# Kernel tuning notes

Hardware: AMD Instinct MI355X
Metric: run time of the kernel (lower is better)

The kernel has to match this reference:

```python
import jax, jax.numpy as jnp
import numpy as np

HID = 128   # hidden_size
EDGE = 16   # edge_size
L = 3       # n_layers
K = 3       # sparse_k
U = 4       # atoms per block (uniform)
NB = 20000  # number of blocks
N = NB * U  # number of atoms
EB = 30000  # number of block-level edges


def _egnn_forward(H, Z, edges, edge_attr,
                  emb_in_w, emb_in_b, emb_out_w, emb_out_b,
                  edge_w1, edge_b1, edge_w2, edge_b2,
                  node_w1, node_b1, node_w2, node_b2,
                  coord_w1, coord_b1, coord_w2):
    # ---- sparse-k atom edges from block edges (uniform U atoms per block) ----
    off = jnp.arange(U)
    src_atoms = edges[0][:, None] * U + off            # [EB, U]
    dst_atoms = edges[1][:, None] * U + off            # [EB, U]
    # squared distances between every src/dst atom pair of each block edge
    d2 = jnp.sum((Z[src_atoms][:, :, None, :] - Z[dst_atoms][:, None, :, :]) ** 2, -1)  # [EB,U,U]
    _, idx = jax.lax.top_k(-d2, K)                     # K nearest dst atoms per src atom
    row = jnp.broadcast_to(src_atoms[:, :, None], (EB, U, K)).reshape(-1)   # [E]
    col = jnp.take_along_axis(jnp.broadcast_to(dst_atoms[:, None, :], (EB, U, U)), idx, axis=2).reshape(-1)
    edge_id = jnp.broadcast_to(jnp.arange(EB)[:, None, None], (EB, U, K)).reshape(-1)
    eattr = edge_attr[edge_id]                         # gather block-edge attr per atom edge [E, EDGE]

    # ---- EGNN (Satorras egnn_clean: SiLU, residual h, mean coord agg) ----
    h = H @ emb_in_w + emb_in_b
    x = Z
    ones = jnp.ones((row.shape[0], 1), Z.dtype)
    cnt = jnp.clip(jax.ops.segment_sum(ones, row, num_segments=N), 1.0)
    for l in range(L):
        diff = x[row] - x[col]                         # [E,3]
        radial = jnp.sum(diff * diff, -1, keepdims=True)
        m = jnp.concatenate([h[row], h[col], radial, eattr], -1)   # [E, 2*HID+1+EDGE]
        m = jax.nn.silu(m @ edge_w1[l] + edge_b1[l])
        m = jax.nn.silu(m @ edge_w2[l] + edge_b2[l])   # edge messages [E, HID]
        # coordinate update (mean aggregation over outgoing edges of row)
        w = jax.nn.silu(m @ coord_w1[l] + coord_b1[l]) @ coord_w2[l]   # [E,1]
        x = x + jax.ops.segment_sum(diff * w, row, num_segments=N) / cnt
        # node update (sum aggregation, residual)
        agg = jax.ops.segment_sum(m, row, num_segments=N)
        hn = jnp.concatenate([h, agg], -1)
        h = h + (jax.nn.silu(hn @ node_w1[l] + node_b1[l]) @ node_w2[l] + node_b2[l])
    h = h @ emb_out_w + emb_out_b
    return h, x


def setup_inputs() -> dict:
    key = jax.random.key(0)
    ks = jax.random.split(key, 16)
    s = 0.05
    p = {}
    p["H"] = jax.random.normal(ks[0], (N, HID), jnp.float32)
    p["Z"] = jax.random.normal(ks[1], (N, 3), jnp.float32) * 3.0
    p["block_id"] = jnp.repeat(jnp.arange(NB, dtype=jnp.int32), U)
    p["batch_id"] = jnp.zeros((N,), jnp.int32)
    p["edges"] = jax.random.randint(ks[2], (2, EB), 0, NB, dtype=jnp.int32)
    p["edge_attr"] = jax.random.normal(ks[3], (EB, EDGE), jnp.float32)
    p["emb_in_w"] = jax.random.normal(ks[4], (HID, HID), jnp.float32) * s
    p["emb_in_b"] = jnp.zeros((HID,), jnp.float32)
    p["emb_out_w"] = jax.random.normal(ks[5], (HID, HID), jnp.float32) * s
    p["emb_out_b"] = jnp.zeros((HID,), jnp.float32)
    p["edge_w1"] = jax.random.normal(ks[6], (L, 2 * HID + 1 + EDGE, HID), jnp.float32) * s
    p["edge_b1"] = jnp.zeros((L, HID), jnp.float32)
    p["edge_w2"] = jax.random.normal(ks[7], (L, HID, HID), jnp.float32) * s
    p["edge_b2"] = jnp.zeros((L, HID), jnp.float32)
    p["node_w1"] = jax.random.normal(ks[8], (L, 2 * HID, HID), jnp.float32) * s
    p["node_b1"] = jnp.zeros((L, HID), jnp.float32)
    p["node_w2"] = jax.random.normal(ks[9], (L, HID, HID), jnp.float32) * s
    p["node_b2"] = jnp.zeros((L, HID), jnp.float32)
    p["coord_w1"] = jax.random.normal(ks[10], (L, HID, HID), jnp.float32) * s
    p["coord_b1"] = jnp.zeros((L, HID), jnp.float32)
    p["coord_w2"] = jax.random.normal(ks[11], (L, HID, 1), jnp.float32) * s
    return p


def reference(H, Z, block_id, batch_id, edges, edge_attr,
              emb_in_w, emb_in_b, emb_out_w, emb_out_b,
              edge_w1, edge_b1, edge_w2, edge_b2,
              node_w1, node_b1, node_w2, node_b2,
              coord_w1, coord_b1, coord_w2):
    # block_id / batch_id are carried for API fidelity; uniform-U block layout is static.
    return _egnn_forward(H, Z, edges, edge_attr,
                         emb_in_w, emb_in_b, emb_out_w, emb_out_b,
                         edge_w1, edge_b1, edge_w2, edge_b2,
                         node_w1, node_b1, node_w2, node_b2,
                         coord_w1, coord_b1, coord_w2)
```

## Files before the change

### kernel.cpp

```cpp
#include <hip/hip_runtime.h>
#include <math.h>

#define HIDC 128
#define EDGEF 16
#define LAY 3
#define KNN 3
#define UU 4
#define NBLK 20000
#define NATOM (NBLK*UU)
#define EBK 30000
#define EALL (EBK*UU*KNN)
#define NGRP (EBK*UU)

#define W1F_L 36864
#define W2F_L 16384
#define NW1F_L 32768

#define E_WG 16
#define ROWS_WG (E_WG*12)
#define WAVES_WG 12

typedef __attribute__((ext_vector_type(8))) short bf16x8;
typedef __attribute__((ext_vector_type(4))) float f32x4;

__device__ __forceinline__ float silu_f(float v) {
    return __fdividef(v, 1.0f + __expf(-v));
}

__device__ __forceinline__ unsigned short f2bf(float f) {
    union { float f; unsigned int u; } v; v.f = f;
    unsigned int r = v.u + 0x7FFFu + ((v.u >> 16) & 1u);
    return (unsigned short)(r >> 16);
}

__device__ __forceinline__ float bf2f(unsigned short h) {
    union { unsigned int u; float f; } t; t.u = ((unsigned int)h) << 16;
    return t.f;
}

__device__ __forceinline__ void split2(float v, short& hi, short& lo) {
    unsigned short h = f2bf(v);
    hi = (short)h;
    lo = (short)f2bf(v - bf2f(h));
}

__device__ __forceinline__ void csplit(float v, unsigned short& hi, unsigned short& lo) {
    unsigned int hu = __float_as_uint(v) & 0xffff0000u;
    hi = (unsigned short)(hu >> 16);
    lo = f2bf(v - __uint_as_float(hu));
}

__device__ __forceinline__ unsigned int cvtpk2(float a, float b) {
    unsigned int r;
    asm("v_cvt_pk_bf16_f32 %0, %1, %2" : "=v"(r) : "v"(a), "v"(b));
    return r;
}

__device__ __forceinline__ void stage16(const unsigned short* gsrc, unsigned short* ldst) {
    __builtin_amdgcn_global_load_lds(
        (const __attribute__((address_space(1))) unsigned int*)(const void*)gsrc,
        (__attribute__((address_space(3))) unsigned int*)(void*)ldst,
        16, 0, 0);
}


__global__ void k_count(const int* __restrict__ edges, int* __restrict__ degB) {
    int e = blockIdx.x * 256 + threadIdx.x;
    if (e < EBK) atomicAdd(&degB[edges[e]], 1);
}

__global__ void k_scan(const int* __restrict__ degB, int* __restrict__ offB) {
    __shared__ int s[1024];
    __shared__ int carry;
    if (threadIdx.x == 0) carry = 0;
    __syncthreads();
    for (int base = 0; base < NBLK; base += 1024) {
        int i = base + threadIdx.x;
        int v = (i < NBLK) ? degB[i] : 0;
        s[threadIdx.x] = v;
        __syncthreads();
        for (int d = 1; d < 1024; d <<= 1) {
            int t = (threadIdx.x >= d) ? s[threadIdx.x - d] : 0;
            __syncthreads();
            s[threadIdx.x] += t;
            __syncthreads();
        }
        if (i < NBLK) offB[i] = carry + s[threadIdx.x] - v;
        int tot = s[1023];
        __syncthreads();
        if (threadIdx.x == 0) carry += tot;
        __syncthreads();
    }
    if (threadIdx.x == 0) offB[NBLK] = carry;
}

__global__ void k_fill(const int* __restrict__ edges, const int* __restrict__ offB,
                       int* __restrict__ cursor, int* __restrict__ listE) {
    int e = blockIdx.x * 256 + threadIdx.x;
    if (e < EBK) {
        int b = edges[e];
        int p = atomicAdd(&cursor[b], 1);
        listE[offB[b] + p] = e;
    }
}

__global__ void k_topk(const int* __restrict__ edges, const float* __restrict__ Z,
                       int* __restrict__ colIdx) {
    int t = blockIdx.x * 256 + threadIdx.x;
    if (t >= EBK * UU) return;
    int e = t >> 2, u = t & 3;
    int b0 = edges[e], b1 = edges[EBK + e];
    int s = b0 * UU + u;
    float zs0 = Z[s*3+0], zs1 = Z[s*3+1], zs2 = Z[s*3+2];
    float d2[UU];
    #pragma unroll
    for (int v = 0; v < UU; v++) {
        int d = b1 * UU + v;
        float a0 = __fsub_rn(zs0, Z[d*3+0]);
        float a1 = __fsub_rn(zs1, Z[d*3+1]);
        float a2 = __fsub_rn(zs2, Z[d*3+2]);
        float p0 = __fmul_rn(a0, a0);
        float p1 = __fmul_rn(a1, a1);
        float p2 = __fmul_rn(a2, a2);
        d2[v] = __fadd_rn(__fadd_rn(p0, p1), p2);
    }
    bool used[UU] = {false, false, false, false};
    #pragma unroll
    for (int k = 0; k < KNN; k++) {
        int best = -1;
        float bd = INFINITY;
        #pragma unroll
        for (int v = 0; v < UU; v++) {
            if (!used[v] && d2[v] < bd) { bd = d2[v]; best = v; }
        }
        used[best] = true;
        colIdx[t * KNN + k] = b1 * UU + best;
    }
}


__global__ void k_wfrag(const float* __restrict__ ew1, const float* __restrict__ ew2,
                        const float* __restrict__ cw1,
                        const float* __restrict__ nw1, const float* __restrict__ nw2,
                        unsigned short* __restrict__ w1f_hi, unsigned short* __restrict__ w1f_lo,
                        unsigned short* __restrict__ w2f_hi, unsigned short* __restrict__ w2f_lo,
                        unsigned short* __restrict__ c1f_hi, unsigned short* __restrict__ c1f_lo,
                        unsigned short* __restrict__ n1f_hi, unsigned short* __restrict__ n1f_lo,
                        unsigned short* __restrict__ n2f_hi, unsigned short* __restrict__ n2f_lo) {
    int i = blockIdx.x * 256 + threadIdx.x;
    float v = 0.f;
    unsigned short* dh = nullptr;
    unsigned short* dl = nullptr;
    int di = 0;
    if (i < 3 * W1F_L) {
        int l = i / W1F_L, rem = i % W1F_L;
        int chunk = rem >> 9, lane = (rem >> 3) & 63, t = rem & 7;
        int kb = chunk >> 3, j = chunk & 7;
        int k = kb*32 + (lane >> 4)*8 + t, n = j*16 + (lane & 15);
        v = (k < 273) ? ew1[(size_t)l*273*128 + (size_t)k*128 + n] : 0.f;
        dh = w1f_hi; dl = w1f_lo; di = i;
    } else {
        int i2 = i - 3 * W1F_L;
        if (i2 < 3 * W2F_L) {
            int l = i2 / W2F_L, rem = i2 % W2F_L;
            int chunk = rem >> 9, lane = (rem >> 3) & 63, t = rem & 7;
            int kb = chunk >> 3, j = chunk & 7;
            int k = kb*32 + (lane >> 4)*8 + t, n = j*16 + (lane & 15);
            v = ew2[(size_t)l*128*128 + (size_t)k*128 + n];
            dh = w2f_hi; dl = w2f_lo; di = i2;
        } else {
            int i3 = i2 - 3 * W2F_L;
            if (i3 < 3 * W2F_L) {
                int l = i3 / W2F_L, rem = i3 % W2F_L;
                int chunk = rem >> 9, lane = (rem >> 3) & 63, t = rem & 7;
                int kb = chunk >> 3, j = chunk & 7;
                int k = kb*32 + (lane >> 4)*8 + t, n = j*16 + (lane & 15);
                v = cw1[(size_t)l*128*128 + (size_t)k*128 + n];
                dh = c1f_hi; dl = c1f_lo; di = i3;
            } else {
                int i4 = i3 - 3 * W2F_L;
                if (i4 < 3 * NW1F_L) {
                    int l = i4 / NW1F_L, rem = i4 % NW1F_L;
                    int chunk = rem >> 9, lane = (rem >> 3) & 63, t = rem & 7;
                    int kb = chunk >> 3, j = chunk & 7;
                    int k = kb*32 + (lane >> 4)*8 + t, n = j*16 + (lane & 15);
                    v = nw1[(size_t)l*256*128 + (size_t)k*128 + n];
                    dh = n1f_hi; dl = n1f_lo; di = i4;
                } else {
                    int i5 = i4 - 3 * NW1F_L;
                    if (i5 >= 3 * W2F_L) return;
                    int l = i5 / W2F_L, rem = i5 % W2F_L;
                    int chunk = rem >> 9, lane = (rem >> 3) & 63, t = rem & 7;
                    int kb = chunk >> 3, j = chunk & 7;
                    int k = kb*32 + (lane >> 4)*8 + t, n = j*16 + (lane & 15);
                    v = nw2[(size_t)l*128*128 + (size_t)k*128 + n];
                    dh = n2f_hi; dl = n2f_lo; di = i5;
                }
            }
        }
    }
    short hi, lo;
    split2(v, hi, lo);
    dh[di] = (unsigned short)hi;
    dl[di] = (unsigned short)lo;
}


__global__ __launch_bounds__(768, 6) void k_edge_flat(
    const unsigned short* __restrict__ hHI,
    const unsigned short* __restrict__ hLO,
    const float* __restrict__ x,
    const float* __restrict__ eattr,
    const int* __restrict__ edges0,
    const int* __restrict__ colIdx,
    const unsigned short* __restrict__ w1f_hi, const unsigned short* __restrict__ w1f_lo,
    const unsigned short* __restrict__ w2f_hi, const unsigned short* __restrict__ w2f_lo,
    const unsigned short* __restrict__ c1f_hi, const unsigned short* __restrict__ c1f_lo,
    const float* __restrict__ eb1,
    const float* __restrict__ eb2,
    const float* __restrict__ cb1,
    const float* __restrict__ cw2v,
    unsigned short* __restrict__ msum,
    float* __restrict__ xsum)
{
    __shared__ unsigned short wbufH[4096], wbufL[4096];
    __shared__ unsigned short Mlds[ROWS_WG * 128];
    __shared__ float diffLDS[ROWS_WG][3];
    __shared__ float pLDS[ROWS_WG];

    const int tid = threadIdx.x;
    const int wid = tid >> 6, l = tid & 63;
    const int g = l >> 4, er = l & 15;
    const int e_base = blockIdx.x * E_WG;
    const int r0 = wid * 16;

    const int row_g = r0 + er;
    const int e_loc = row_g / 12;
    const int rr = row_g - e_loc * 12;
    const int u = rr / 3;
    const int kk = rr - u * 3;
    const int e = e_base + e_loc;
    const int bs = edges0[e];
    const int srcA = bs * 4 + u;
    const int colA = colIdx[(e * 4 + u) * 3 + kk];
    float rad = 0.f;
    if (g == 0) {
        float dx = x[srcA*3+0] - x[colA*3+0];
        float dy = x[srcA*3+1] - x[colA*3+1];
        float dz = x[srcA*3+2] - x[colA*3+2];
        rad = dx*dx + dy*dy + dz*dz;
        diffLDS[row_g][0] = dx; diffLDS[row_g][1] = dy; diffLDS[row_g][2] = dz;
    }

    const int goff = wid * 512 + l * 8;
    unsigned short* lb0H = wbufH + wid * 512;
    unsigned short* lb1H = wbufH + 2048 + wid * 512;
    unsigned short* lb0L = wbufL + wid * 512;
    unsigned short* lb1L = wbufL + 2048 + wid * 512;

    {
        f32x4 acc[8];
        #pragma unroll
        for (int jj = 0; jj < 8; jj++) acc[jj] = (f32x4){0.f, 0.f, 0.f, 0.f};

        #pragma unroll 1
        for (int kb = 0; kb < 9; kb++) {
            __syncthreads();
            if (wid < 4) {
                stage16(w1f_hi + (kb << 12) + goff,        lb0H);
                stage16(w1f_hi + (kb << 12) + 2048 + goff, lb1H);
                stage16(w1f_lo + (kb << 12) + goff,        lb0L);
                stage16(w1f_lo + (kb << 12) + 2048 + goff, lb1L);
            }
            bf16x8 ah, al;
            if (kb < 8) {
                const size_t off = (kb < 4) ? ((size_t)srcA * 128 + kb * 32 + g * 8)
                                            : ((size_t)colA * 128 + (kb - 4) * 32 + g * 8);
                ah = *(const bf16x8*)(hHI + off);
                al = *(const bf16x8*)(hLO + off);
            } else {
                float tv[8];
                #pragma unroll
                for (int q = 0; q < 8; q++) tv[q] = 0.f;
                if (g == 0) {
                    tv[0] = rad;
                    #pragma unroll
                    for (int q = 1; q < 8; q++) tv[q] = eattr[(size_t)e*16 + (q-1)];
                } else if (g == 1) {
                    #pragma unroll
                    for (int q = 0; q < 8; q++) tv[q] = eattr[(size_t)e*16 + 7 + q];
                } else if (g == 2) {
                    tv[0] = eattr[(size_t)e*16 + 15];
                }
                #pragma unroll
                for (int q = 0; q < 8; q++) { unsigned short hh, ll; csplit(tv[q], hh, ll); ah[q] = (short)hh; al[q] = (short)ll; }
            }
            __syncthreads();
            __builtin_amdgcn_s_setprio(1);
            #pragma unroll
            for (int jj = 0; jj < 8; jj++) {
                const int off = (jj << 9) + (l << 3);
                bf16x8 wh = *(const bf16x8*)&wbufH[off];
                bf16x8 wl = *(const bf16x8*)&wbufL[off];
                acc[jj] = __builtin_amdgcn_mfma_f32_16x16x32_bf16(ah, wh, acc[jj], 0, 0, 0);
                acc[jj] = __builtin_amdgcn_mfma_f32_16x16x32_bf16(al, wh, acc[jj], 0, 0, 0);
                acc[jj] = __builtin_amdgcn_mfma_f32_16x16x32_bf16(ah, wl, acc[jj], 0, 0, 0);
            }
            __builtin_amdgcn_s_setprio(0);
        }
        #pragma unroll
        for (int jp = 0; jp < 4; jp++) {
            const int n0 = (jp * 2) * 16 + er, n1 = n0 + 16;
            const float b0 = eb1[n0], b1 = eb1[n1];
            #pragma unroll
            for (int reg = 0; reg < 4; reg++) {
                const int row = r0 + g * 4 + reg;
                float v0 = silu_f(acc[jp*2][reg] + b0);
                float v1 = silu_f(acc[jp*2+1][reg] + b1);
                unsigned int pk = cvtpk2(v0, v1);
                const int m = (row & 7) << 3;
                Mlds[row * 128 + (n0 ^ m)] = (unsigned short)pk;
                Mlds[row * 128 + (n1 ^ m)] = (unsigned short)(pk >> 16);
            }
        }
    }

    {
        f32x4 acc[8];
        #pragma unroll
        for (int jj = 0; jj < 8; jj++) acc[jj] = (f32x4){0.f, 0.f, 0.f, 0.f};

        #pragma unroll 1
        for (int kb = 0; kb < 4; kb++) {
            __syncthreads();
            if (wid < 4) {
                stage16(w2f_hi + (kb << 12) + goff,        lb0H);
                stage16(w2f_hi + (kb << 12) + 2048 + goff, lb1H);
                stage16(w2f_lo + (kb << 12) + goff,        lb0L);
                stage16(w2f_lo + (kb << 12) + 2048 + goff, lb1L);
            }
            const int aoff = row_g * 128 + ((kb * 32 + g * 8) ^ ((row_g & 7) << 3));
            bf16x8 a2 = *(const bf16x8*)&Mlds[aoff];
            __syncthreads();
            __builtin_amdgcn_s_setprio(1);
            #pragma unroll
            for (int jj = 0; jj < 8; jj++) {
                const int off = (jj << 9) + (l << 3);
                bf16x8 wh = *(const bf16x8*)&wbufH[off];
                bf16x8 wl = *(const bf16x8*)&wbufL[off];
                acc[jj] = __builtin_amdgcn_mfma_f32_16x16x32_bf16(a2, wh, acc[jj], 0, 0, 0);
                acc[jj] = __builtin_amdgcn_mfma_f32_16x16x32_bf16(a2, wl, acc[jj], 0, 0, 0);
            }
            __builtin_amdgcn_s_setprio(0);
        }
        #pragma unroll
        for (int jp = 0; jp < 4; jp++) {
            const int n0 = (jp * 2) * 16 + er, n1 = n0 + 16;
            const float b0 = eb2[n0], b1 = eb2[n1];
            #pragma unroll
            for (int reg = 0; reg < 4; reg++) {
                const int row = r0 + g * 4 + reg;
                float v0 = silu_f(acc[jp*2][reg] + b0);
                float v1 = silu_f(acc[jp*2+1][reg] + b1);
                unsigned int pk = cvtpk2(v0, v1);
                const int m = (row & 7) << 3;
                Mlds[row * 128 + (n0 ^ m)] = (unsigned short)pk;
                Mlds[row * 128 + (n1 ^ m)] = (unsigned short)(pk >> 16);
            }
        }
    }

    {
        f32x4 acc[8];
        #pragma unroll
        for (int jj = 0; jj < 8; jj++) acc[jj] = (f32x4){0.f, 0.f, 0.f, 0.f};

        #pragma unroll 1
        for (int kb = 0; kb < 4; kb++) {
            __syncthreads();
            if (wid < 4) {
                stage16(c1f_hi + (kb << 12) + goff,        lb0H);
                stage16(c1f_hi + (kb << 12) + 2048 + goff, lb1H);
                stage16(c1f_lo + (kb << 12) + goff,        lb0L);
                stage16(c1f_lo + (kb << 12) + 2048 + goff, lb1L);
            }
            const int aoff = row_g * 128 + ((kb * 32 + g * 8) ^ ((row_g & 7) << 3));
            bf16x8 a3 = *(const bf16x8*)&Mlds[aoff];
            __syncthreads();
            __builtin_amdgcn_s_setprio(1);
            #pragma unroll
            for (int jj = 0; jj < 8; jj++) {
                const int off = (jj << 9) + (l << 3);
                bf16x8 wh = *(const bf16x8*)&wbufH[off];
                bf16x8 wl = *(const bf16x8*)&wbufL[off];
                acc[jj] = __builtin_amdgcn_mfma_f32_16x16x32_bf16(a3, wh, acc[jj], 0, 0, 0);
                acc[jj] = __builtin_amdgcn_mfma_f32_16x16x32_bf16(a3, wl, acc[jj], 0, 0, 0);
            }
            __builtin_amdgcn_s_setprio(0);
        }
        float p[4] = {0.f, 0.f, 0.f, 0.f};
        #pragma unroll
        for (int jj = 0; jj < 8; jj++) {
            const int n = jj * 16 + er;
            const float cb = cb1[n], cw = cw2v[n];
            #pragma unroll
            for (int reg = 0; reg < 4; reg++)
                p[reg] += silu_f(acc[jj][reg] + cb) * cw;
        }
        #pragma unroll
        for (int d = 1; d < 16; d <<= 1) {
            #pragma unroll
            for (int reg = 0; reg < 4; reg++)
                p[reg] += __shfl_xor(p[reg], d);
        }
        if (er == 0) {
            #pragma unroll
            for (int reg = 0; reg < 4; reg++)
                pLDS[r0 + g * 4 + reg] = p[reg];
        }
    }
    __syncthreads();

    for (int t = tid; t < E_WG * 4 * 64; t += 768) {
        const int gi = t >> 6, cp = t & 63;
        const int c0 = cp * 2;
        const int el = gi >> 2, uu2 = gi & 3;
        const int base = el * 12 + uu2 * 3;
        float s0 = 0.f, s1 = 0.f;
        #pragma unroll
        for (int k3 = 0; k3 < 3; k3++) {
            const int row = base + k3;
            const int m = (row & 7) << 3;
            unsigned int pr = *(const unsigned int*)&Mlds[row * 128 + (c0 ^ m)];
            s0 += bf2f((unsigned short)(pr & 0xffffu));
            s1 += bf2f((unsigned short)(pr >> 16));
        }
        ((unsigned int*)msum)[(size_t)((e_base + el) * 4 + uu2) * 64 + cp] = cvtpk2(s0, s1);
    }
    if (tid < E_WG * 4 * 3) {
        const int gi = tid / 3, c = tid - gi * 3;
        const int el = gi >> 2, uu2 = gi & 3;
        const int base = el * 12 + uu2 * 3;
        float xs = 0.f;
        #pragma unroll
        for (int k3 = 0; k3 < 3; k3++)
            xs += diffLDS[base + k3][c] * pLDS[base + k3];
        xsum[(size_t)((e_base + el) * 4 + uu2) * 3 + c] = xs;
    }
}


__global__ void k_xupd(const float* __restrict__ xcur, const float* __restrict__ xsum,
                       const int* __restrict__ offB, const int* __restrict__ listE,
                       float* __restrict__ xnext)
{
    int i = blockIdx.x * 256 + threadIdx.x;
    if (i >= NATOM * 3) return;
    int a = i / 3, d = i - a * 3;
    int b = a >> 2, u = a & 3;
    int o0 = offB[b], o1 = offB[b + 1];
    float xs = 0.f;
    for (int pos = o0; pos < o1; pos++) {
        int e = listE[pos];
        xs += xsum[(size_t)(e * 4 + u) * 3 + d];
    }
    int deg = o1 - o0;
    xnext[i] = xcur[i] + ((deg > 0) ? xs / (3.0f * (float)deg) : 0.f);
}


__global__ __launch_bounds__(256, 4) void k_node(
    unsigned short* __restrict__ hHI,
    unsigned short* __restrict__ hLO,
    const unsigned short* __restrict__ msum,
    const int* __restrict__ offB,
    const int* __restrict__ listE,
    const unsigned short* __restrict__ n1f_hi, const unsigned short* __restrict__ n1f_lo,
    const unsigned short* __restrict__ n2f_hi, const unsigned short* __restrict__ n2f_lo,
    const float* __restrict__ nb1,
    const float* __restrict__ nb2)
{
    __shared__ unsigned short wbufH[4096], wbufL[4096];
    __shared__ unsigned short hid[4][16 * 128];

    const int tid = threadIdx.x;
    const int wid = tid >> 6, l = tid & 63;
    const int g = l >> 4, er = l & 15;
    const int a0 = blockIdx.x * 64 + wid * 16;
    const int a = a0 + er;
    const int b = a >> 2, u = a & 3;
    const int o0 = offB[b], o1 = offB[b + 1];

    const int goff = wid * 512 + l * 8;
    unsigned short* lb0H = wbufH + wid * 512;
    unsigned short* lb1H = wbufH + 2048 + wid * 512;
    unsigned short* lb0L = wbufL + wid * 512;
    unsigned short* lb1L = wbufL + 2048 + wid * 512;

    {
        f32x4 acc[8];
        #pragma unroll
        for (int jj = 0; jj < 8; jj++) acc[jj] = (f32x4){0.f, 0.f, 0.f, 0.f};

        #pragma unroll 1
        for (int kb = 0; kb < 8; kb++) {
            __syncthreads();
            stage16(n1f_hi + (kb << 12) + goff,        lb0H);
            stage16(n1f_hi + (kb << 12) + 2048 + goff, lb1H);
            stage16(n1f_lo + (kb << 12) + goff,        lb0L);
            stage16(n1f_lo + (kb << 12) + 2048 + goff, lb1L);
            bf16x8 ah, al;
            if (kb < 4) {
                const size_t off = (size_t)a * 128 + kb * 32 + g * 8;
                ah = *(const bf16x8*)(hHI + off);
                al = *(const bf16x8*)(hLO + off);
            } else {
                float s[8];
                #pragma unroll
                for (int q = 0; q < 8; q++) s[q] = 0.f;
                for (int pos = o0; pos < o1; pos++) {
                    const int e = listE[pos];
                    bf16x8 mv = *(const bf16x8*)(msum + (size_t)(e * 4 + u) * 128 + (kb - 4) * 32 + g * 8);
                    #pragma unroll
                    for (int q = 0; q < 8; q++) s[q] += bf2f((unsigned short)mv[q]);
                }
                #pragma unroll
                for (int q = 0; q < 8; q++) { unsigned short hh, ll; csplit(s[q], hh, ll); ah[q] = (short)hh; al[q] = (short)ll; }
            }
            __syncthreads();
            __builtin_amdgcn_s_setprio(1);
            #pragma unroll
            for (int jj = 0; jj < 8; jj++) {
                const int off = (jj << 9) + (l << 3);
                bf16x8 wh = *(const bf16x8*)&wbufH[off];
                bf16x8 wl = *(const bf16x8*)&wbufL[off];
                acc[jj] = __builtin_amdgcn_mfma_f32_16x16x32_bf16(ah, wh, acc[jj], 0, 0, 0);
                acc[jj] = __builtin_amdgcn_mfma_f32_16x16x32_bf16(al, wh, acc[jj], 0, 0, 0);
                acc[jj] = __builtin_amdgcn_mfma_f32_16x16x32_bf16(ah, wl, acc[jj], 0, 0, 0);
            }
            __builtin_amdgcn_s_setprio(0);
        }
        #pragma unroll
        for (int jp = 0; jp < 4; jp++) {
            const int n0 = (jp * 2) * 16 + er, n1 = n0 + 16;
            const float b0 = nb1[n0], b1 = nb1[n1];
            #pragma unroll
            for (int reg = 0; reg < 4; reg++) {
                const int row = g * 4 + reg;
                float v0 = silu_f(acc[jp*2][reg] + b0);
                float v1 = silu_f(acc[jp*2+1][reg] + b1);
                unsigned int pk = cvtpk2(v0, v1);
                const int m = (row & 7) << 3;
                hid[wid][row * 128 + (n0 ^ m)] = (unsigned short)pk;
                hid[wid][row * 128 + (n1 ^ m)] = (unsigned short)(pk >> 16);
            }
        }
    }

    {
        f32x4 acc[8];
        #pragma unroll
        for (int jj = 0; jj < 8; jj++) acc[jj] = (f32x4){0.f, 0.f, 0.f, 0.f};

        #pragma unroll 1
        for (int kb = 0; kb < 4; kb++) {
            __syncthreads();
            stage16(n2f_hi + (kb << 12) + goff,        lb0H);
            stage16(n2f_hi + (kb << 12) + 2048 + goff, lb1H);
            stage16(n2f_lo + (kb << 12) + goff,        lb0L);
            stage16(n2f_lo + (kb << 12) + 2048 + goff, lb1L);
            const int aoff = er * 128 + ((kb * 32 + g * 8) ^ ((er & 7) << 3));
            bf16x8 ab = *(const bf16x8*)&hid[wid][aoff];
            __syncthreads();
            __builtin_amdgcn_s_setprio(1);
            #pragma unroll
            for (int jj = 0; jj < 8; jj++) {
                const int off = (jj << 9) + (l << 3);
                bf16x8 wh = *(const bf16x8*)&wbufH[off];
                bf16x8 wl = *(const bf16x8*)&wbufL[off];
                acc[jj] = __builtin_amdgcn_mfma_f32_16x16x32_bf16(ab, wh, acc[jj], 0, 0, 0);
                acc[jj] = __builtin_amdgcn_mfma_f32_16x16x32_bf16(ab, wl, acc[jj], 0, 0, 0);
            }
            __builtin_amdgcn_s_setprio(0);
        }
        #pragma unroll
        for (int jj = 0; jj < 8; jj++) {
            const int n = jj * 16 + er;
            const float bv = nb2[n];
            #pragma unroll
            for (int reg = 0; reg < 4; reg++) {
                const int row = g * 4 + reg;
                const size_t idx = (size_t)(a0 + row) * 128 + n;
                float v = acc[jj][reg] + bv + bf2f(hHI[idx]) + bf2f(hLO[idx]);
                unsigned short hh, ll; csplit(v, hh, ll);
                hHI[idx] = hh;
                hLO[idx] = ll;
            }
        }
    }
}


template<bool PLANEIN, bool PLANEOUT>
__global__ __launch_bounds__(128) void k_gemm(
    const float* __restrict__ A0,
    const unsigned short* __restrict__ AHI, const unsigned short* __restrict__ ALO,
    const float* __restrict__ W, const float* __restrict__ bias,
    float* __restrict__ C,
    unsigned short* __restrict__ CHI, unsigned short* __restrict__ CLO, int M)
{
    __shared__ float At[128][32];
    __shared__ float Bs[32][128];
    const int tid = threadIdx.x;
    const int tile0 = blockIdx.x * 32;
    const int r = tid >> 2, part = tid & 3;
    const int gr = tile0 + r;

    if (gr < M) {
        #pragma unroll
        for (int j = 0; j < 8; j++) {
            int c = part * 32 + j * 4;
            float f0, f1, f2, f3;
            if (PLANEIN) {
                ushort4 vh = *(const ushort4*)(AHI + (size_t)gr * 128 + c);
                ushort4 vl = *(const ushort4*)(ALO + (size_t)gr * 128 + c);
                f0 = bf2f(vh.x) + bf2f(vl.x);
                f1 = bf2f(vh.y) + bf2f(vl.y);
                f2 = bf2f(vh.z) + bf2f(vl.z);
                f3 = bf2f(vh.w) + bf2f(vl.w);
            } else {
                float4 v = *(const float4*)(A0 + (size_t)gr * 128 + c);
                f0 = v.x; f1 = v.y; f2 = v.z; f3 = v.w;
            }
            At[c][r] = f0; At[c+1][r] = f1; At[c+2][r] = f2; At[c+3][r] = f3;
        }
    } else {
        #pragma unroll
        for (int j = 0; j < 8; j++) {
            int c = part * 32 + j * 4;
            At[c][r] = 0.f; At[c+1][r] = 0.f; At[c+2][r] = 0.f; At[c+3][r] = 0.f;
        }
    }

    float acc[4][8];
    #pragma unroll
    for (int i = 0; i < 4; i++)
        #pragma unroll
        for (int j = 0; j < 8; j++) acc[i][j] = 0.f;

    const int tx = tid & 15, ty = tid >> 4;

    for (int kb = 0; kb < 4; kb++) {
        __syncthreads();
        #pragma unroll
        for (int j = 0; j < 8; j++) {
            int li = j * 512 + tid * 4;
            int kk = li >> 7, c = li & 127;
            float4 v = *(const float4*)(W + (size_t)(kb * 32 + kk) * 128 + c);
            *(float4*)&Bs[kk][c] = v;
        }
        __syncthreads();
        #pragma unroll 8
        for (int kk = 0; kk < 32; kk++) {
            float4 a  = *(const float4*)&At[kb * 32 + kk][ty * 4];
            float4 b0 = *(const float4*)&Bs[kk][tx * 8];
            float4 b1 = *(const float4*)&Bs[kk][tx * 8 + 4];
            float av[4] = {a.x, a.y, a.z, a.w};
            float bv[8] = {b0.x, b0.y, b0.z, b0.w, b1.x, b1.y, b1.z, b1.w};
            #pragma unroll
            for (int i = 0; i < 4; i++)
                #pragma unroll
                for (int j = 0; j < 8; j++)
                    acc[i][j] = fmaf(av[i], bv[j], acc[i][j]);
        }
    }

    #pragma unroll
    for (int i = 0; i < 4; i++) {
        int grr = tile0 + ty * 4 + i;
        if (grr >= M) continue;
        #pragma unroll
        for (int j = 0; j < 8; j++) {
            int c = tx * 8 + j;
            float v = acc[i][j] + bias[c];
            if (PLANEOUT) {
                unsigned short hh, ll; csplit(v, hh, ll);
                CHI[(size_t)grr * 128 + c] = hh;
                CLO[(size_t)grr * 128 + c] = ll;
            } else {
                C[(size_t)grr * 128 + c] = v;
            }
        }
    }
}


extern "C" void kernel_launch(void* const* d_in, const int* in_sizes, int n_in,
                              void* d_out, int out_size, void* d_ws, size_t ws_size,
                              hipStream_t stream) {
    const float* H        = (const float*)d_in[0];
    const float* Z        = (const float*)d_in[1];
    const int*   edges    = (const int*)  d_in[4];
    const float* eattr    = (const float*)d_in[5];
    const float* emb_in_w = (const float*)d_in[6];
    const float* emb_in_b = (const float*)d_in[7];
    const float* emb_out_w= (const float*)d_in[8];
    const float* emb_out_b= (const float*)d_in[9];
    const float* edge_w1  = (const float*)d_in[10];
    const float* edge_b1  = (const float*)d_in[11];
    const float* edge_w2  = (const float*)d_in[12];
    const float* edge_b2  = (const float*)d_in[13];
    const float* node_w1  = (const float*)d_in[14];
    const float* node_b1  = (const float*)d_in[15];
    const float* node_w2  = (const float*)d_in[16];
    const float* node_b2  = (const float*)d_in[17];
    const float* coord_w1 = (const float*)d_in[18];
    const float* coord_b1 = (const float*)d_in[19];
    const float* coord_w2 = (const float*)d_in[20];

    float* out  = (float*)d_out;
    float* hbuf = out;
    float* xout = out + (size_t)NATOM * 128;

    char* w = (char*)d_ws;
    unsigned short* hHI = (unsigned short*)w;  w += (size_t)NATOM * 128 * 2;
    unsigned short* hLO = (unsigned short*)w;  w += (size_t)NATOM * 128 * 2;
    unsigned short* msum = (unsigned short*)w; w += (size_t)NGRP * 128 * 2;
    float* xsum = (float*)w;           w += (size_t)NGRP * 3 * 4;
    float* xA  = (float*)w;            w += (size_t)NATOM * 3 * 4;
    float* xB  = (float*)w;            w += (size_t)NATOM * 3 * 4;
    unsigned short* w1f_hi = (unsigned short*)w;  w += (size_t)3 * W1F_L * 2;
    unsigned short* w1f_lo = (unsigned short*)w;  w += (size_t)3 * W1F_L * 2;
    unsigned short* w2f_hi = (unsigned short*)w;  w += (size_t)3 * W2F_L * 2;
    unsigned short* w2f_lo = (unsigned short*)w;  w += (size_t)3 * W2F_L * 2;
    unsigned short* c1f_hi = (unsigned short*)w;  w += (size_t)3 * W2F_L * 2;
    unsigned short* c1f_lo = (unsigned short*)w;  w += (size_t)3 * W2F_L * 2;
    unsigned short* n1f_hi = (unsigned short*)w;  w += (size_t)3 * NW1F_L * 2;
    unsigned short* n1f_lo = (unsigned short*)w;  w += (size_t)3 * NW1F_L * 2;
    unsigned short* n2f_hi = (unsigned short*)w;  w += (size_t)3 * W2F_L * 2;
    unsigned short* n2f_lo = (unsigned short*)w;  w += (size_t)3 * W2F_L * 2;
    int* colIdx = (int*)w;             w += (size_t)EALL * 4;
    int* degB   = (int*)w;             w += (size_t)NBLK * 4;
    int* cursor = (int*)w;             w += (size_t)NBLK * 4;
    int* listE  = (int*)w;             w += (size_t)EBK * 4;
    int* offB   = (int*)w;             w += (size_t)(NBLK + 1) * 4;

    hipMemsetAsync(degB,   0, NBLK * sizeof(int), stream);
    hipMemsetAsync(cursor, 0, NBLK * sizeof(int), stream);

    k_count<<<(EBK + 255) / 256, 256, 0, stream>>>(edges, degB);
    k_scan <<<1, 1024, 0, stream>>>(degB, offB);
    k_fill <<<(EBK + 255) / 256, 256, 0, stream>>>(edges, offB, cursor, listE);
    k_topk <<<(EBK * UU + 255) / 256, 256, 0, stream>>>(edges, Z, colIdx);

    {
        int total = 3 * W1F_L + 3 * W2F_L + 3 * W2F_L + 3 * NW1F_L + 3 * W2F_L;
        k_wfrag<<<(total + 255) / 256, 256, 0, stream>>>(
            edge_w1, edge_w2, coord_w1, node_w1, node_w2,
            w1f_hi, w1f_lo, w2f_hi, w2f_lo, c1f_hi, c1f_lo,
            n1f_hi, n1f_lo, n2f_hi, n2f_lo);
    }

    k_gemm<false, true><<<NATOM / 32, 128, 0, stream>>>(
        H, nullptr, nullptr, emb_in_w, emb_in_b, nullptr, hHI, hLO, NATOM);

    const float* xcur = Z;
    for (int l = 0; l < LAY; l++) {
        float* xnext = (l == 0) ? xA : (l == 1) ? xB : xout;

        k_edge_flat<<<EBK / E_WG, 768, 0, stream>>>(
            hHI, hLO, xcur, eattr, edges, colIdx,
            w1f_hi + (size_t)l * W1F_L, w1f_lo + (size_t)l * W1F_L,
            w2f_hi + (size_t)l * W2F_L, w2f_lo + (size_t)l * W2F_L,
            c1f_hi + (size_t)l * W2F_L, c1f_lo + (size_t)l * W2F_L,
            edge_b1 + l * 128, edge_b2 + l * 128, coord_b1 + l * 128, coord_w2 + l * 128,
            msum, xsum);

        k_xupd<<<(NATOM * 3 + 255) / 256, 256, 0, stream>>>(xcur, xsum, offB, listE, xnext);

        k_node<<<NATOM / 64, 256, 0, stream>>>(
            hHI, hLO, msum, offB, listE,
            n1f_hi + (size_t)l * NW1F_L, n1f_lo + (size_t)l * NW1F_L,
            n2f_hi + (size_t)l * W2F_L, n2f_lo + (size_t)l * W2F_L,
            node_b1 + l * 128, node_b2 + l * 128);

        xcur = xnext;
    }

    k_gemm<true, false><<<NATOM / 32, 128, 0, stream>>>(
        nullptr, hHI, hLO, emb_out_w, emb_out_b, hbuf, nullptr, nullptr, NATOM);
}
```

Measured before the change: 918.7 us.

## Widen node kernel to 12 waves sharing staged weights; vectorize gemm I/O

The node-update kernel now runs 768 threads per block covering 192 atoms, so each weight tile staged into LDS by four waves is reused by twelve waves instead of four, cutting global weight traffic per atom. Tail atoms are bounds-guarded and the hidden activation buffer becomes one shared array. Separately, the dense gemm kernel loads inputs in 8-wide vectors and writes hi/lo bf16 output planes with packed 128-bit stores instead of scalar stores. The larger LDS footprint and block size may reduce how many blocks fit per CU.

```diff
diff --git a/kernel.cpp b/kernel.cpp
--- a/kernel.cpp
+++ b/kernel.cpp
@@ -18,7 +18,7 @@
 
 #define E_WG 16
 #define ROWS_WG (E_WG*12)
-#define WAVES_WG 12
+#define NODE_ROWS 192
 
 typedef __attribute__((ext_vector_type(8))) short bf16x8;
 typedef __attribute__((ext_vector_type(4))) float f32x4;
@@ -469,7 +469,7 @@
 }
 
 
-__global__ __launch_bounds__(256, 4) void k_node(
+__global__ __launch_bounds__(768, 6) void k_node(
     unsigned short* __restrict__ hHI,
     unsigned short* __restrict__ hLO,
     const unsigned short* __restrict__ msum,
@@ -481,15 +481,19 @@
     const float* __restrict__ nb2)
 {
     __shared__ unsigned short wbufH[4096], wbufL[4096];
-    __shared__ unsigned short hid[4][16 * 128];
+    __shared__ unsigned short hid[NODE_ROWS * 128];
 
     const int tid = threadIdx.x;
     const int wid = tid >> 6, l = tid & 63;
     const int g = l >> 4, er = l & 15;
-    const int a0 = blockIdx.x * 64 + wid * 16;
-    const int a = a0 + er;
-    const int b = a >> 2, u = a & 3;
-    const int o0 = offB[b], o1 = offB[b + 1];
+    const int r0 = wid * 16;
+    const int row_g = r0 + er;
+    const int a = blockIdx.x * NODE_ROWS + row_g;
+    const bool aOK = (a < NATOM);
+    const int aC = aOK ? a : 0;
+    const int b = aC >> 2, u = aC & 3;
+    const int o0 = aOK ? offB[b] : 0;
+    const int o1 = aOK ? offB[b + 1] : 0;
 
     const int goff = wid * 512 + l * 8;
     unsigned short* lb0H = wbufH + wid * 512;
@@ -505,13 +509,15 @@
         #pragma unroll 1
         for (int kb = 0; kb < 8; kb++) {
             __syncthreads();
-            stage16(n1f_hi + (kb << 12) + goff,        lb0H);
-            stage16(n1f_hi + (kb << 12) + 2048 + goff, lb1H);
-            stage16(n1f_lo + (kb << 12) + goff,        lb0L);
-            stage16(n1f_lo + (kb << 12) + 2048 + goff, lb1L);
+            if (wid < 4) {
+                stage16(n1f_hi + (kb << 12) + goff,        lb0H);
+                stage16(n1f_hi + (kb << 12) + 2048 + goff, lb1H);
+                stage16(n1f_lo + (kb << 12) + goff,        lb0L);
+                stage16(n1f_lo + (kb << 12) + 2048 + goff, lb1L);
+            }
             bf16x8 ah, al;
             if (kb < 4) {
-                const size_t off = (size_t)a * 128 + kb * 32 + g * 8;
+                const size_t off = (size_t)aC * 128 + kb * 32 + g * 8;
                 ah = *(const bf16x8*)(hHI + off);
                 al = *(const bf16x8*)(hLO + off);
             } else {
@@ -546,13 +552,13 @@
             const float b0 = nb1[n0], b1 = nb1[n1];
             #pragma unroll
             for (int reg = 0; reg < 4; reg++) {
-                const int row = g * 4 + reg;
+                const int row = r0 + g * 4 + reg;
                 float v0 = silu_f(acc[jp*2][reg] + b0);
                 float v1 = silu_f(acc[jp*2+1][reg] + b1);
                 unsigned int pk = cvtpk2(v0, v1);
                 const int m = (row & 7) << 3;
-                hid[wid][row * 128 + (n0 ^ m)] = (unsigned short)pk;
-                hid[wid][row * 128 + (n1 ^ m)] = (unsigned short)(pk >> 16);
+                hid[row * 128 + (n0 ^ m)] = (unsigned short)pk;
+                hid[row * 128 + (n1 ^ m)] = (unsigned short)(pk >> 16);
             }
         }
     }
@@ -565,12 +571,14 @@
         #pragma unroll 1
         for (int kb = 0; kb < 4; kb++) {
             __syncthreads();
-            stage16(n2f_hi + (kb << 12) + goff,        lb0H);
-            stage16(n2f_hi + (kb << 12) + 2048 + goff, lb1H);
-            stage16(n2f_lo + (kb << 12) + goff,        lb0L);
-            stage16(n2f_lo + (kb << 12) + 2048 + goff, lb1L);
-            const int aoff = er * 128 + ((kb * 32 + g * 8) ^ ((er & 7) << 3));
-            bf16x8 ab = *(const bf16x8*)&hid[wid][aoff];
+            if (wid < 4) {
+                stage16(n2f_hi + (kb << 12) + goff,        lb0H);
+                stage16(n2f_hi + (kb << 12) + 2048 + goff, lb1H);
+                stage16(n2f_lo + (kb << 12) + goff,        lb0L);
+                stage16(n2f_lo + (kb << 12) + 2048 + goff, lb1L);
+            }
+            const int aoff = row_g * 128 + ((kb * 32 + g * 8) ^ ((row_g & 7) << 3));
+            bf16x8 ab = *(const bf16x8*)&hid[aoff];
             __syncthreads();
             __builtin_amdgcn_s_setprio(1);
             #pragma unroll
@@ -589,12 +597,15 @@
             const float bv = nb2[n];
             #pragma unroll
             for (int reg = 0; reg < 4; reg++) {
-                const int row = g * 4 + reg;
-                const size_t idx = (size_t)(a0 + row) * 128 + n;
-                float v = acc[jj][reg] + bv + bf2f(hHI[idx]) + bf2f(hLO[idx]);
-                unsigned short hh, ll; csplit(v, hh, ll);
-                hHI[idx] = hh;
-                hLO[idx] = ll;
+                const int row = r0 + g * 4 + reg;
+                const int aw = blockIdx.x * NODE_ROWS + row;
+                if (aw < NATOM) {
+                    const size_t idx = (size_t)aw * 128 + n;
+                    float v = acc[jj][reg] + bv + bf2f(hHI[idx]) + bf2f(hLO[idx]);
+                    unsigned short hh, ll; csplit(v, hh, ll);
+                    hHI[idx] = hh;
+                    hLO[idx] = ll;
+                }
             }
         }
     }
@@ -618,21 +629,20 @@
 
     if (gr < M) {
         #pragma unroll
-        for (int j = 0; j < 8; j++) {
-            int c = part * 32 + j * 4;
-            float f0, f1, f2, f3;
+        for (int j2 = 0; j2 < 4; j2++) {
+            int c = part * 32 + j2 * 8;
             if (PLANEIN) {
-                ushort4 vh = *(const ushort4*)(AHI + (size_t)gr * 128 + c);
-                ushort4 vl = *(const ushort4*)(ALO + (size_t)gr * 128 + c);
-                f0 = bf2f(vh.x) + bf2f(vl.x);
-                f1 = bf2f(vh.y) + bf2f(vl.y);
-                f2 = bf2f(vh.z) + bf2f(vl.z);
-                f3 = bf2f(vh.w) + bf2f(vl.w);
+                bf16x8 vh = *(const bf16x8*)(AHI + (size_t)gr * 128 + c);
+                bf16x8 vl = *(const bf16x8*)(ALO + (size_t)gr * 128 + c);
+                #pragma unroll
+                for (int q = 0; q < 8; q++)
+                    At[c + q][r] = bf2f((unsigned short)vh[q]) + bf2f((unsigned short)vl[q]);
             } else {
-                float4 v = *(const float4*)(A0 + (size_t)gr * 128 + c);
-                f0 = v.x; f1 = v.y; f2 = v.z; f3 = v.w;
-            }
-            At[c][r] = f0; At[c+1][r] = f1; At[c+2][r] = f2; At[c+3][r] = f3;
+                float4 v0 = *(const float4*)(A0 + (size_t)gr * 128 + c);
+                float4 v1 = *(const float4*)(A0 + (size_t)gr * 128 + c + 4);
+                At[c][r] = v0.x; At[c+1][r] = v0.y; At[c+2][r] = v0.z; At[c+3][r] = v0.w;
+                At[c+4][r] = v1.x; At[c+5][r] = v1.y; At[c+6][r] = v1.z; At[c+7][r] = v1.w;
+            }
         }
     } else {
         #pragma unroll
@@ -675,21 +685,32 @@
         }
     }
 
+    const int c0 = tx * 8;
     #pragma unroll
     for (int i = 0; i < 4; i++) {
         int grr = tile0 + ty * 4 + i;
         if (grr >= M) continue;
-        #pragma unroll
-        for (int j = 0; j < 8; j++) {
-            int c = tx * 8 + j;
-            float v = acc[i][j] + bias[c];
-            if (PLANEOUT) {
-                unsigned short hh, ll; csplit(v, hh, ll);
-                CHI[(size_t)grr * 128 + c] = hh;
-                CLO[(size_t)grr * 128 + c] = ll;
-            } else {
-                C[(size_t)grr * 128 + c] = v;
-            }
+        if (PLANEOUT) {
+            float v[8];
+            #pragma unroll
+            for (int j = 0; j < 8; j++) v[j] = acc[i][j] + bias[c0 + j];
+            unsigned int hw[4], lw[4];
+            #pragma unroll
+            for (int q = 0; q < 4; q++) {
+                float a0 = v[2*q], a1 = v[2*q+1];
+                unsigned int ua = __float_as_uint(a0) & 0xffff0000u;
+                unsigned int ub = __float_as_uint(a1) & 0xffff0000u;
+                hw[q] = (ua >> 16) | ub;
+                lw[q] = cvtpk2(a0 - __uint_as_float(ua), a1 - __uint_as_float(ub));
+            }
+            uint4 hv = {hw[0], hw[1], hw[2], hw[3]};
+            uint4 lv = {lw[0], lw[1], lw[2], lw[3]};
+            *(uint4*)(CHI + (size_t)grr * 128 + c0) = hv;
+            *(uint4*)(CLO + (size_t)grr * 128 + c0) = lv;
+        } else {
+            #pragma unroll
+            for (int j = 0; j < 8; j++)
+                C[(size_t)grr * 128 + c0 + j] = acc[i][j] + bias[c0 + j];
         }
     }
 }
@@ -778,7 +799,7 @@
 
         k_xupd<<<(NATOM * 3 + 255) / 256, 256, 0, stream>>>(xcur, xsum, offB, listE, xnext);
 
-        k_node<<<NATOM / 64, 256, 0, stream>>>(
+        k_node<<<(NATOM + NODE_ROWS - 1) / NODE_ROWS, 768, 0, stream>>>(
             hHI, hLO, msum, offB, listE,
             n1f_hi + (size_t)l * NW1F_L, n1f_lo + (size_t)l * NW1F_L,
             n2f_hi + (size_t)l * W2F_L, n2f_lo + (size_t)l * W2F_L,
```

Result: faster. 892.1 us (-2.9%).
